# Kernel tuning notes

Hardware: AMD Instinct MI355X
Metric: run time of the kernel (lower is better)

## Reference

```python
import jax, jax.numpy as jnp
import numpy as np

N, C1, C2, H, W, NH = 4, 512, 512, 32, 32, 8


def _conv(x, w, pad):
    return jax.lax.conv_general_dilated(
        x, w, window_strides=(1, 1), padding=[(pad, pad), (pad, pad)],
        dimension_numbers=("NCHW", "OIHW", "NCHW"))


def _heads(t, n, c, nh):
    # [n, c, h, w] -> [n, nh, c, hw//nh] (spatial dim split across heads)
    return jnp.transpose(t.reshape(n, c, nh, -1), (0, 2, 1, 3))


def _attend(q, k, v):
    # q:[n,nh,Sq,d] k,v:[n,nh,Sk,d]; fp32 math as in the original
    scale = 1.0 / np.sqrt(k.shape[-1])
    att = jnp.einsum("nhqd,nhkd->nhqk", q.astype(jnp.float32), k.astype(jnp.float32)) * scale
    att = jax.nn.softmax(att, axis=-1)
    return jnp.einsum("nhqk,nhkd->nhqd", att, v.astype(jnp.float32))


def setup_inputs() -> dict:
    key = jax.random.key(0)
    ks = jax.random.split(key, 11)
    s = 0.02
    inp = {
        "x_l": jax.random.normal(ks[0], (N, C1, H, W), jnp.float32),
        "x_g": jax.random.normal(ks[1], (N, C2, H, W), jnp.float32),
        "Wk1": jax.random.normal(ks[2], (C1, C1, 3, 3), jnp.float32) * s,
        "Wq1": jax.random.normal(ks[3], (C1, C1, 3, 3), jnp.float32) * s,
        "Wv1": jax.random.normal(ks[4], (C1, C1, 3, 3), jnp.float32) * s,
        "Wk2": jax.random.normal(ks[5], (C2, C2, 3, 3), jnp.float32) * s,
        "Wq2": jax.random.normal(ks[6], (C2, C2, 3, 3), jnp.float32) * s,
        "Wv2": jax.random.normal(ks[7], (C2, C2, 3, 3), jnp.float32) * s,
        "Wp1": jax.random.normal(ks[8], (C1, C1, 1, 1), jnp.float32) * s,
        "Wp2": jax.random.normal(ks[9], (C2, C2, 1, 1), jnp.float32) * s,
        "resweight": jnp.ones((), jnp.float32),  # init 0 in torch; 1 used so the branch is active
    }
    return inp


def reference(x_l, x_g, Wk1, Wq1, Wv1, Wk2, Wq2, Wv2, Wp1, Wp2, resweight):
    n, c1, h, w = x_l.shape
    c2 = x_g.shape[1]
    k_l = _heads(_conv(x_l, Wk1, 1), n, c1, NH)
    q_l = _heads(_conv(x_l, Wq1, 1), n, c1, NH)
    v_l = _heads(_conv(x_l, Wv1, 1), n, c1, NH)
    k_g = _heads(_conv(x_g, Wk2, 1), n, c2, NH)
    q_g = _heads(_conv(x_g, Wq2, 1), n, c2, NH)
    v_g = _heads(_conv(x_g, Wv2, 1), n, c2, NH)

    # global queries attend over local keys/values
    y_g = _attend(q_g, k_l, v_l)                       # [n, nh, c2, hw/nh]
    y_g = jnp.transpose(y_g, (0, 2, 1, 3)).reshape(n, c2, h, w)
    y_g = _conv(y_g, Wp2, 0)

    # local queries attend over global keys/values
    y_l = _attend(q_l, k_g, v_g)                       # [n, nh, c1, hw/nh]
    y_l = jnp.transpose(y_l, (0, 2, 1, 3)).reshape(n, c1, h, w)
    y_l = _conv(y_l, Wp1, 0)

    return (x_l + y_l * resweight, x_g + y_g * resweight)
```

## Files before the change

kernel.cpp:

```cpp
#include <hip/hip_runtime.h>
#include <hip/hip_bf16.h>
#include <stdint.h>

typedef unsigned short u16;
typedef unsigned int u32;

#define TSLOT 2097152
#define IC_ELEMS 37748736ull
#define WB_ELEMS 14155776ull

typedef __attribute__((ext_vector_type(8))) short short8;
typedef __attribute__((ext_vector_type(8))) unsigned short u16x8;
typedef __attribute__((ext_vector_type(4))) float f32x4;

__device__ __forceinline__ float bf2f(u16 u) {
    union { u32 i; float f; } v; v.i = ((u32)u) << 16; return v.f;
}
__device__ __forceinline__ u16 f2bf(float f) {
    union { u32 i; float f; } v; v.f = f;
    u32 u = v.i;
    return (u16)((u + 0x7FFFu + ((u >> 16) & 1u)) >> 16);
}
__device__ __forceinline__ u32 pkbf(float a, float b) {
    __hip_bfloat162 h = __float22bfloat162_rn(make_float2(a, b));
    u32 u; __builtin_memcpy(&u, &h, 4); return u;
}

__device__ __forceinline__ void gl_lds16(const u16* g, u16* l) {
    __builtin_amdgcn_global_load_lds(
        (const __attribute__((address_space(1))) void*)(uintptr_t)(const void*)g,
        (__attribute__((address_space(3))) void*)(uintptr_t)(void*)l,
        16, 0, 0);
}

__global__ __launch_bounds__(256) void wconv_prep(
    const float* __restrict__ w0, const float* __restrict__ w1,
    const float* __restrict__ w2, const float* __restrict__ w3,
    const float* __restrict__ w4, const float* __restrict__ w5,
    u16* __restrict__ wbf)
{
    const int tsr = blockIdx.y;
    const float* src = tsr == 0 ? w0 : tsr == 1 ? w1 : tsr == 2 ? w2
                     : tsr == 3 ? w3 : tsr == 4 ? w4 : w5;
    const size_t base = (size_t)blockIdx.x * 4096 + threadIdx.x * 16;
    u16* dst = wbf + (size_t)tsr * 2359296 + base;
    const float4* s4 = (const float4*)(src + base);
    float4 f0 = s4[0], f1 = s4[1], f2 = s4[2], f3 = s4[3];
    u32 p[4];
    p[0] = pkbf(f0.x, f0.y); p[1] = pkbf(f0.z, f0.w);
    p[2] = pkbf(f1.x, f1.y); p[3] = pkbf(f1.z, f1.w);
    *(uint4*)dst = *(uint4*)p;
    p[0] = pkbf(f2.x, f2.y); p[1] = pkbf(f2.z, f2.w);
    p[2] = pkbf(f3.x, f3.y); p[3] = pkbf(f3.z, f3.w);
    *(uint4*)(dst + 8) = *(uint4*)p;
}

__global__ __launch_bounds__(256) void im2col_prep(
    const float* __restrict__ xl, const float* __restrict__ xg,
    u16* __restrict__ ic)
{
    __shared__ float xs[32][4][32];

    const int t  = threadIdx.x;
    const int mt = blockIdx.x;
    const int ct = blockIdx.y;
    const int m0 = mt * 64;
    const int img  = m0 >> 12;
    const int m_in = m0 & 4095;
    const int n_i  = m_in >> 10;
    const int y0   = (m_in & 1023) >> 5;

    const float* xp = (img ? xg : xl) + ((size_t)n_i * 512 + ct * 32) * 1024;

    for (int v = t; v < 4096; v += 256) {
        int ci = v >> 7;
        int r  = (v >> 5) & 3;
        int xx = v & 31;
        int yy = y0 - 1 + r;
        xs[ci][r][xx] = ((unsigned)yy < 32u) ? xp[ci * 1024 + yy * 32 + xx] : 0.f;
    }
    __syncthreads();

    const int m_local = t >> 2;
    const int q       = t & 3;
    const int y_sel   = m_local >> 5;
    const int x       = m_local & 31;
    u16* orow = ic + (size_t)(m0 + m_local) * 4608 + (size_t)(ct * 32 + q * 8) * 9;

    #pragma unroll
    for (int c = 0; c < 9; ++c) {
        u16x8 st;
        #pragma unroll
        for (int u = 0; u < 8; ++u) {
            const int e   = c * 8 + u;
            const int cil = q * 8 + e / 9;
            const int tap = e % 9;
            const int ky  = tap / 3, kx = tap % 3;
            int xx = x + kx - 1;
            float v = ((unsigned)xx < 32u) ? xs[cil][y_sel + ky][xx] : 0.f;
            st[u] = f2bf(v);
        }
        *(u16x8*)(orow + c * 8) = st;
    }
}

__global__ __launch_bounds__(256) void conv_gemm(
    const u16* __restrict__ ic, const u16* __restrict__ wbf,
    u16* __restrict__ kl, u16* __restrict__ ql, u16* __restrict__ vl,
    u16* __restrict__ kg, u16* __restrict__ qg, u16* __restrict__ vg)
{
    __shared__ u16 A_lds[128 * 64];
    __shared__ u16 B_lds[128 * 64];

    const int t  = threadIdx.x;
    const int mt = blockIdx.x;
    const int nt = blockIdx.y;
    const int img = mt >> 5;
    const int wt  = nt >> 2;
    const int co0 = (nt & 3) * 128;
    const int m0  = mt * 128;

    u16* osel = img == 0 ? (wt == 0 ? kl : wt == 1 ? ql : vl)
                         : (wt == 0 ? kg : wt == 1 ? qg : vg);
    const u16* wsel = wbf + (size_t)(img * 3 + wt) * 2359296;

    const int lane = t & 63;
    const int w4   = t >> 6;

    const int s_rb  = w4 * 8 + (lane >> 3);
    const int s_col = ((lane & 7) ^ (lane >> 3)) * 8;
    const u16* agp[4];
    const u16* bgp[4];
    #pragma unroll
    for (int i = 0; i < 4; ++i) {
        agp[i] = ic   + (size_t)(m0  + s_rb + i * 32) * 4608 + s_col;
        bgp[i] = wsel + (size_t)(co0 + s_rb + i * 32) * 4608 + s_col;
    }
    u16* Adst = A_lds + w4 * 512;
    u16* Bdst = B_lds + w4 * 512;

    const int wm = (w4 & 1) * 64;
    const int wn = (w4 >> 1) * 64;
    const int fr = lane & 15;
    const int qd = lane >> 4;
    int arow[4], brow[4];
    #pragma unroll
    for (int i = 0; i < 4; ++i) {
        arow[i] = wm + i * 16 + fr;
        brow[i] = wn + i * 16 + fr;
    }

    f32x4 acc[4][4] = {};

    for (int kb = 0; kb < 4608; kb += 64) {
        __syncthreads();
        #pragma unroll
        for (int i = 0; i < 4; ++i) {
            gl_lds16(agp[i] + kb, Adst + i * 2048);
            gl_lds16(bgp[i] + kb, Bdst + i * 2048);
        }
        __syncthreads();
        #pragma unroll
        for (int ks = 0; ks < 2; ++ks) {
            short8 af[4], bq[4];
            #pragma unroll
            for (int i = 0; i < 4; ++i) {
                int c = (ks * 4 + qd) ^ (arow[i] & 7);
                af[i] = *(const short8*)&A_lds[arow[i] * 64 + c * 8];
            }
            #pragma unroll
            for (int j = 0; j < 4; ++j) {
                int c = (ks * 4 + qd) ^ (brow[j] & 7);
                bq[j] = *(const short8*)&B_lds[brow[j] * 64 + c * 8];
            }
            #pragma unroll
            for (int i = 0; i < 4; ++i)
                #pragma unroll
                for (int j = 0; j < 4; ++j)
                    acc[i][j] = __builtin_amdgcn_mfma_f32_16x16x32_bf16(
                        af[i], bq[j], acc[i][j], 0, 0, 0);
        }
    }

    const int m_in = m0 & 4095;
    const int n_i  = m_in >> 10;
    const int head = (m_in & 1023) >> 7;
    u16* ob = osel + (size_t)(n_i * 8 + head) * 65536;
    if (wt == 2) {
        #pragma unroll
        for (int i = 0; i < 4; ++i) {
            int dd0 = wm + i * 16 + qd * 4;
            #pragma unroll
            for (int j = 0; j < 4; ++j) {
                int co = co0 + wn + j * 16 + fr;
                #pragma unroll
                for (int r = 0; r < 4; ++r)
                    ob[(size_t)(dd0 + r) * 512 + co] = f2bf(acc[i][j][r]);
            }
        }
    } else {
        #pragma unroll
        for (int i = 0; i < 4; ++i) {
            int dd0 = wm + i * 16 + qd * 4;
            #pragma unroll
            for (int j = 0; j < 4; ++j) {
                int co = co0 + wn + j * 16 + fr;
                ushort4 st;
                st.x = f2bf(acc[i][j][0]); st.y = f2bf(acc[i][j][1]);
                st.z = f2bf(acc[i][j][2]); st.w = f2bf(acc[i][j][3]);
                *(ushort4*)(ob + (size_t)co * 128 + dd0) = st;
            }
        }
    }
}

__global__ __launch_bounds__(256) void attn_mfma(
    const u16* __restrict__ Q0, const u16* __restrict__ K0,
    const u16* __restrict__ V0, u16* __restrict__ O0,
    const u16* __restrict__ Q1, const u16* __restrict__ K1,
    const u16* __restrict__ V1, u16* __restrict__ O1)
{
    __shared__ u16 Qs[64][136];
    __shared__ u16 Ks[64][136];
    __shared__ u16 Vs[128][72];
    __shared__ u16 Ps[64][72];

    const int t    = threadIdx.x;
    const int lane = t & 63;
    const int w    = t >> 6;
    const int qt   = blockIdx.x;
    const int nh   = blockIdx.y;
    const int z    = blockIdx.z;

    const u16* Q = (z ? Q1 : Q0) + (size_t)nh * 65536;
    const u16* K = (z ? K1 : K0) + (size_t)nh * 65536;
    const u16* V = (z ? V1 : V0) + (size_t)nh * 65536;
    u16*       O = (z ? O1 : O0) + (size_t)nh * 65536;

    const int q0 = qt * 64;
    for (int v = t; v < 1024; v += 256) {
        int row = v >> 4, c8 = (v & 15) * 8;
        *(u16x8*)&Qs[row][c8] = *(const u16x8*)(Q + (size_t)(q0 + row) * 128 + c8);
    }

    const int fr  = lane & 15;
    const int qd  = lane >> 4;
    const int koq = qd * 8;

    float m_run[4] = {-3e38f, -3e38f, -3e38f, -3e38f};
    float l_run[4] = {0.f, 0.f, 0.f, 0.f};
    f32x4 Ot[8] = {};
    const float scale = 0.08838834764831845f;

    for (int cb = 0; cb < 8; ++cb) {
        __syncthreads();
        const int kb = cb * 64;
        for (int v = t; v < 1024; v += 256) {
            int row = v >> 4, c8 = (v & 15) * 8;
            *(u16x8*)&Ks[row][c8] = *(const u16x8*)(K + (size_t)(kb + row) * 128 + c8);
        }
        for (int v = t; v < 1024; v += 256) {
            int row = v >> 3, c8 = (v & 7) * 8;
            *(u16x8*)&Vs[row][c8] = *(const u16x8*)(V + (size_t)row * 512 + kb + c8);
        }
        __syncthreads();

        f32x4 s[4] = {};
        #pragma unroll
        for (int dstep = 0; dstep < 4; ++dstep) {
            short8 a = *(const short8*)&Qs[w * 16 + fr][dstep * 32 + koq];
            #pragma unroll
            for (int nj = 0; nj < 4; ++nj) {
                short8 b = *(const short8*)&Ks[nj * 16 + fr][dstep * 32 + koq];
                s[nj] = __builtin_amdgcn_mfma_f32_16x16x32_bf16(a, b, s[nj], 0, 0, 0);
            }
        }

        float al[4];
        #pragma unroll
        for (int r = 0; r < 4; ++r) {
            float mc = fmaxf(fmaxf(s[0][r], s[1][r]), fmaxf(s[2][r], s[3][r])) * scale;
            mc = fmaxf(mc, __shfl_xor(mc, 1));
            mc = fmaxf(mc, __shfl_xor(mc, 2));
            mc = fmaxf(mc, __shfl_xor(mc, 4));
            mc = fmaxf(mc, __shfl_xor(mc, 8));
            float mn = fmaxf(m_run[r], mc);
            al[r] = __expf(m_run[r] - mn);
            m_run[r] = mn;
            float rs = 0.f;
            #pragma unroll
            for (int nj = 0; nj < 4; ++nj) {
                float p = __expf(s[nj][r] * scale - mn);
                s[nj][r] = p;
                rs += p;
            }
            rs += __shfl_xor(rs, 1);
            rs += __shfl_xor(rs, 2);
            rs += __shfl_xor(rs, 4);
            rs += __shfl_xor(rs, 8);
            l_run[r] = l_run[r] * al[r] + rs;
        }

        #pragma unroll
        for (int nj = 0; nj < 4; ++nj)
            #pragma unroll
            for (int r = 0; r < 4; ++r)
                Ps[w * 16 + qd * 4 + r][nj * 16 + fr] = f2bf(s[nj][r]);

        {
            int srcl = (fr >> 2) << 4;
            float a0 = __shfl(al[0], srcl), a1 = __shfl(al[1], srcl);
            float a2 = __shfl(al[2], srcl), a3 = __shfl(al[3], srcl);
            int rsel = fr & 3;
            float ac = rsel == 0 ? a0 : rsel == 1 ? a1 : rsel == 2 ? a2 : a3;
            #pragma unroll
            for (int t8 = 0; t8 < 8; ++t8)
                #pragma unroll
                for (int r = 0; r < 4; ++r)
                    Ot[t8][r] *= ac;
        }

        #pragma unroll
        for (int ks = 0; ks < 2; ++ks) {
            short8 b = *(const short8*)&Ps[w * 16 + fr][ks * 32 + koq];
            #pragma unroll
            for (int t8 = 0; t8 < 8; ++t8) {
                short8 a = *(const short8*)&Vs[t8 * 16 + fr][ks * 32 + koq];
                Ot[t8] = __builtin_amdgcn_mfma_f32_16x16x32_bf16(a, b, Ot[t8], 0, 0, 0);
            }
        }
    }

    int srcl = (fr >> 2) << 4;
    float l0 = __shfl(l_run[0], srcl), l1 = __shfl(l_run[1], srcl);
    float l2 = __shfl(l_run[2], srcl), l3 = __shfl(l_run[3], srcl);
    int rsel = fr & 3;
    float lc = rsel == 0 ? l0 : rsel == 1 ? l1 : rsel == 2 ? l2 : l3;
    float linv = 1.0f / lc;
    int c = q0 + w * 16 + fr;
    #pragma unroll
    for (int t8 = 0; t8 < 8; ++t8)
        #pragma unroll
        for (int r = 0; r < 4; ++r) {
            int d = t8 * 16 + qd * 4 + r;
            O[(size_t)d * 512 + c] = f2bf(Ot[t8][r] * linv);
        }
}

__global__ __launch_bounds__(256) void proj_mfma(
    const float* __restrict__ Wp1, const float* __restrict__ Wp2,
    const u16* __restrict__ Otl, const u16* __restrict__ Otg,
    const float* __restrict__ x_l, const float* __restrict__ x_g,
    const float* __restrict__ rwp,
    float* __restrict__ out0, float* __restrict__ out1)
{
    __shared__ u16 A_lds[128][40];
    __shared__ u16 B_lds[128][40];

    const int t  = threadIdx.x;
    const int ct = blockIdx.x;
    const int st = blockIdx.y;
    const int z  = blockIdx.z;
    const int which = z >> 2;
    const int nn    = z & 3;

    const float* Wp = which ? Wp2 : Wp1;
    const u16*   Ot = (which ? Otg : Otl) + (size_t)nn * 524288;
    const float* xr = (which ? x_g : x_l) + (size_t)nn * 524288;
    float*     outp = (which ? out1 : out0) + (size_t)nn * 524288;

    const int co0 = ct * 128, s0 = st * 128;
    const int row = t & 127, half = t >> 7;
    const float* wrow = Wp + (size_t)(co0 + row) * 512 + half * 16;
    const u16*   brow = Ot + (size_t)(s0 + row) * 512 + half * 16;

    const int lane = t & 63;
    const int wv4  = t >> 6;
    const int wm   = (wv4 & 1) * 64;
    const int wn   = (wv4 >> 1) * 64;
    const int fr   = lane & 15;
    const int koq  = (lane >> 4) * 8;

    f32x4 acc[4][4] = {};

    for (int kb = 0; kb < 512; kb += 32) {
        __syncthreads();
        {
            const float4* wp4 = (const float4*)(wrow + kb);
            float4 f0 = wp4[0], f1 = wp4[1], f2 = wp4[2], f3 = wp4[3];
            u32 p[4];
            p[0] = pkbf(f0.x, f0.y); p[1] = pkbf(f0.z, f0.w);
            p[2] = pkbf(f1.x, f1.y); p[3] = pkbf(f1.z, f1.w);
            *(uint4*)&A_lds[row][half * 16] = *(uint4*)p;
            p[0] = pkbf(f2.x, f2.y); p[1] = pkbf(f2.z, f2.w);
            p[2] = pkbf(f3.x, f3.y); p[3] = pkbf(f3.z, f3.w);
            *(uint4*)&A_lds[row][half * 16 + 8] = *(uint4*)p;
        }
        *(u16x8*)&B_lds[row][half * 16]     = *(const u16x8*)(brow + kb);
        *(u16x8*)&B_lds[row][half * 16 + 8] = *(const u16x8*)(brow + kb + 8);
        __syncthreads();
        short8 af[4], bf[4];
        #pragma unroll
        for (int i = 0; i < 4; ++i) af[i] = *(const short8*)&A_lds[wm + i * 16 + fr][koq];
        #pragma unroll
        for (int j = 0; j < 4; ++j) bf[j] = *(const short8*)&B_lds[wn + j * 16 + fr][koq];
        #pragma unroll
        for (int i = 0; i < 4; ++i)
            #pragma unroll
            for (int j = 0; j < 4; ++j)
                acc[i][j] = __builtin_amdgcn_mfma_f32_16x16x32_bf16(af[i], bf[j], acc[i][j], 0, 0, 0);
    }

    const float rwv = *rwp;
    #pragma unroll
    for (int i = 0; i < 4; ++i) {
        int co_b = co0 + wm + i * 16 + (lane >> 4) * 4;
        #pragma unroll
        for (int j = 0; j < 4; ++j) {
            int s = s0 + wn + j * 16 + fr;
            #pragma unroll
            for (int r = 0; r < 4; ++r) {
                size_t a = (size_t)(co_b + r) * 1024 + s;
                outp[a] = xr[a] + rwv * acc[i][j][r];
            }
        }
    }
}

extern "C" void kernel_launch(void* const* d_in, const int* in_sizes, int n_in,
                              void* d_out, int out_size, void* d_ws, size_t ws_size,
                              hipStream_t stream) {
    const float* x_l = (const float*)d_in[0];
    const float* x_g = (const float*)d_in[1];
    const float* Wk1 = (const float*)d_in[2];
    const float* Wq1 = (const float*)d_in[3];
    const float* Wv1 = (const float*)d_in[4];
    const float* Wk2 = (const float*)d_in[5];
    const float* Wq2 = (const float*)d_in[6];
    const float* Wv2 = (const float*)d_in[7];
    const float* Wp1 = (const float*)d_in[8];
    const float* Wp2 = (const float*)d_in[9];
    const float* rw  = (const float*)d_in[10];

    u16* ws  = (u16*)d_ws;
    u16* ic  = ws;
    u16* wbf = ws + IC_ELEMS;
    u16* Kl  = wbf + WB_ELEMS;
    u16* Ql  = Kl  + TSLOT;
    u16* Vtl = Ql  + TSLOT;
    u16* Kg  = Vtl + TSLOT;
    u16* Qg  = Kg  + TSLOT;
    u16* Vtg = Qg  + TSLOT;
    u16* Otg = Vtg + TSLOT;
    u16* Otl = Otg + TSLOT;

    float* out0 = (float*)d_out;
    float* out1 = out0 + (size_t)TSLOT;

    wconv_prep<<<dim3(576, 6), 256, 0, stream>>>(Wk1, Wq1, Wv1, Wk2, Wq2, Wv2, wbf);
    im2col_prep<<<dim3(128, 16), 256, 0, stream>>>(x_l, x_g, ic);

    conv_gemm<<<dim3(64, 12), 256, 0, stream>>>(
        ic, wbf, Kl, Ql, Vtl, Kg, Qg, Vtg);

    attn_mfma<<<dim3(8, 32, 2), 256, 0, stream>>>(
        Qg, Kl, Vtl, Otg, Ql, Kg, Vtg, Otl);

    proj_mfma<<<dim3(4, 8, 8), 256, 0, stream>>>(
        Wp1, Wp2, Otl, Otg, x_l, x_g, rw, out0, out1);
}
```

Measured before the change: 381.1 us.

## Merge prep kernels and use direct global-to-LDS loads in attention and projection

Merges the weight conversion and im2col prep kernels into one launch, and adds a conversion of the projection weights to bf16 there. The attention and projection kernels now stage tiles with global_load_lds into XOR-swizzled LDS layouts instead of register round-trips through padded arrays. The projection K-step doubles to 64. This aims to remove one launch, the in-loop fp32-to-bf16 conversion, and LDS staging overhead. It adds more workspace use and requires the swizzle indexing to be correct.

```diff
diff --git a/kernel.cpp b/kernel.cpp
--- a/kernel.cpp
+++ b/kernel.cpp
@@ -8,6 +8,7 @@
 #define TSLOT 2097152
 #define IC_ELEMS 37748736ull
 #define WB_ELEMS 14155776ull
+#define WPB_ELEMS 524288ull
 
 typedef __attribute__((ext_vector_type(8))) short short8;
 typedef __attribute__((ext_vector_type(8))) unsigned short u16x8;
@@ -33,37 +34,55 @@
         16, 0, 0);
 }
 
-__global__ __launch_bounds__(256) void wconv_prep(
+__global__ __launch_bounds__(256) void prep_all(
+    const float* __restrict__ xl, const float* __restrict__ xg,
     const float* __restrict__ w0, const float* __restrict__ w1,
     const float* __restrict__ w2, const float* __restrict__ w3,
     const float* __restrict__ w4, const float* __restrict__ w5,
-    u16* __restrict__ wbf)
-{
-    const int tsr = blockIdx.y;
-    const float* src = tsr == 0 ? w0 : tsr == 1 ? w1 : tsr == 2 ? w2
-                     : tsr == 3 ? w3 : tsr == 4 ? w4 : w5;
-    const size_t base = (size_t)blockIdx.x * 4096 + threadIdx.x * 16;
-    u16* dst = wbf + (size_t)tsr * 2359296 + base;
-    const float4* s4 = (const float4*)(src + base);
-    float4 f0 = s4[0], f1 = s4[1], f2 = s4[2], f3 = s4[3];
-    u32 p[4];
-    p[0] = pkbf(f0.x, f0.y); p[1] = pkbf(f0.z, f0.w);
-    p[2] = pkbf(f1.x, f1.y); p[3] = pkbf(f1.z, f1.w);
-    *(uint4*)dst = *(uint4*)p;
-    p[0] = pkbf(f2.x, f2.y); p[1] = pkbf(f2.z, f2.w);
-    p[2] = pkbf(f3.x, f3.y); p[3] = pkbf(f3.z, f3.w);
-    *(uint4*)(dst + 8) = *(uint4*)p;
-}
-
-__global__ __launch_bounds__(256) void im2col_prep(
-    const float* __restrict__ xl, const float* __restrict__ xg,
-    u16* __restrict__ ic)
+    const float* __restrict__ wp1, const float* __restrict__ wp2,
+    u16* __restrict__ wbf, u16* __restrict__ ic, u16* __restrict__ wpb)
 {
     __shared__ float xs[32][4][32];
-
-    const int t  = threadIdx.x;
-    const int mt = blockIdx.x;
-    const int ct = blockIdx.y;
+    const int b = blockIdx.x;
+    const int t = threadIdx.x;
+
+    if (b < 3456) {
+        const int tsr = b / 576, inner = b - tsr * 576;
+        const float* src = tsr == 0 ? w0 : tsr == 1 ? w1 : tsr == 2 ? w2
+                         : tsr == 3 ? w3 : tsr == 4 ? w4 : w5;
+        const size_t base = (size_t)inner * 4096 + t * 16;
+        u16* dst = wbf + (size_t)tsr * 2359296 + base;
+        const float4* s4 = (const float4*)(src + base);
+        float4 f0 = s4[0], f1 = s4[1], f2 = s4[2], f3 = s4[3];
+        u32 p[4];
+        p[0] = pkbf(f0.x, f0.y); p[1] = pkbf(f0.z, f0.w);
+        p[2] = pkbf(f1.x, f1.y); p[3] = pkbf(f1.z, f1.w);
+        *(uint4*)dst = *(uint4*)p;
+        p[0] = pkbf(f2.x, f2.y); p[1] = pkbf(f2.z, f2.w);
+        p[2] = pkbf(f3.x, f3.y); p[3] = pkbf(f3.z, f3.w);
+        *(uint4*)(dst + 8) = *(uint4*)p;
+        return;
+    }
+    if (b >= 5504) {
+        const int b3 = b - 5504;
+        const float* src = (b3 < 64) ? wp1 : wp2;
+        const size_t base = (size_t)(b3 & 63) * 4096 + t * 16;
+        u16* dst = wpb + ((b3 < 64) ? 0 : 262144) + base;
+        const float4* s4 = (const float4*)(src + base);
+        float4 f0 = s4[0], f1 = s4[1], f2 = s4[2], f3 = s4[3];
+        u32 p[4];
+        p[0] = pkbf(f0.x, f0.y); p[1] = pkbf(f0.z, f0.w);
+        p[2] = pkbf(f1.x, f1.y); p[3] = pkbf(f1.z, f1.w);
+        *(uint4*)dst = *(uint4*)p;
+        p[0] = pkbf(f2.x, f2.y); p[1] = pkbf(f2.z, f2.w);
+        p[2] = pkbf(f3.x, f3.y); p[3] = pkbf(f3.z, f3.w);
+        *(uint4*)(dst + 8) = *(uint4*)p;
+        return;
+    }
+
+    const int b2 = b - 3456;
+    const int mt = b2 >> 4;
+    const int ct = b2 & 15;
     const int m0 = mt * 64;
     const int img  = m0 >> 12;
     const int m_in = m0 & 4095;
@@ -109,8 +128,8 @@
     u16* __restrict__ kl, u16* __restrict__ ql, u16* __restrict__ vl,
     u16* __restrict__ kg, u16* __restrict__ qg, u16* __restrict__ vg)
 {
-    __shared__ u16 A_lds[128 * 64];
-    __shared__ u16 B_lds[128 * 64];
+    __shared__ __align__(16) u16 A_lds[128 * 64];
+    __shared__ __align__(16) u16 B_lds[128 * 64];
 
     const int t  = threadIdx.x;
     const int mt = blockIdx.x;
@@ -220,9 +239,11 @@
     const u16* __restrict__ Q1, const u16* __restrict__ K1,
     const u16* __restrict__ V1, u16* __restrict__ O1)
 {
-    __shared__ u16 Qs[64][136];
-    __shared__ u16 Ks[64][136];
-    __shared__ u16 Vs[128][72];
+    __shared__ __align__(16) u16 Qlo[64 * 64];
+    __shared__ __align__(16) u16 Qhi[64 * 64];
+    __shared__ __align__(16) u16 Klo[64 * 64];
+    __shared__ __align__(16) u16 Khi[64 * 64];
+    __shared__ __align__(16) u16 Vs[128 * 64];
     __shared__ u16 Ps[64][72];
 
     const int t    = threadIdx.x;
@@ -237,10 +258,20 @@
     const u16* V = (z ? V1 : V0) + (size_t)nh * 65536;
     u16*       O = (z ? O1 : O0) + (size_t)nh * 65536;
 
-    const int q0 = qt * 64;
-    for (int v = t; v < 1024; v += 256) {
-        int row = v >> 4, c8 = (v & 15) * 8;
-        *(u16x8*)&Qs[row][c8] = *(const u16x8*)(Q + (size_t)(q0 + row) * 128 + c8);
+    const int q0    = qt * 64;
+    const int s_rb  = w * 8 + (lane >> 3);
+    const int s_col = ((lane & 7) ^ (lane >> 3)) * 8;
+    u16* const dQl = Qlo + w * 512;
+    u16* const dQh = Qhi + w * 512;
+    u16* const dKl = Klo + w * 512;
+    u16* const dKh = Khi + w * 512;
+    u16* const dV  = Vs  + w * 512;
+
+    #pragma unroll
+    for (int i = 0; i < 2; ++i) {
+        const u16* qr = Q + (size_t)(q0 + s_rb + i * 32) * 128;
+        gl_lds16(qr + s_col,      dQl + i * 2048);
+        gl_lds16(qr + 64 + s_col, dQh + i * 2048);
     }
 
     const int fr  = lane & 15;
@@ -255,23 +286,27 @@
     for (int cb = 0; cb < 8; ++cb) {
         __syncthreads();
         const int kb = cb * 64;
-        for (int v = t; v < 1024; v += 256) {
-            int row = v >> 4, c8 = (v & 15) * 8;
-            *(u16x8*)&Ks[row][c8] = *(const u16x8*)(K + (size_t)(kb + row) * 128 + c8);
-        }
-        for (int v = t; v < 1024; v += 256) {
-            int row = v >> 3, c8 = (v & 7) * 8;
-            *(u16x8*)&Vs[row][c8] = *(const u16x8*)(V + (size_t)row * 512 + kb + c8);
-        }
+        #pragma unroll
+        for (int i = 0; i < 2; ++i) {
+            const u16* kr = K + (size_t)(kb + s_rb + i * 32) * 128;
+            gl_lds16(kr + s_col,      dKl + i * 2048);
+            gl_lds16(kr + 64 + s_col, dKh + i * 2048);
+        }
+        #pragma unroll
+        for (int i = 0; i < 4; ++i)
+            gl_lds16(V + (size_t)(s_rb + i * 32) * 512 + kb + s_col, dV + i * 2048);
         __syncthreads();
 
         f32x4 s[4] = {};
         #pragma unroll
         for (int dstep = 0; dstep < 4; ++dstep) {
-            short8 a = *(const short8*)&Qs[w * 16 + fr][dstep * 32 + koq];
+            const u16* Qh = (dstep < 2) ? Qlo : Qhi;
+            const u16* Kh = (dstep < 2) ? Klo : Khi;
+            const int cq = (((dstep & 1) * 4 + qd) ^ (fr & 7)) * 8;
+            short8 a = *(const short8*)&Qh[(w * 16 + fr) * 64 + cq];
             #pragma unroll
             for (int nj = 0; nj < 4; ++nj) {
-                short8 b = *(const short8*)&Ks[nj * 16 + fr][dstep * 32 + koq];
+                short8 b = *(const short8*)&Kh[(nj * 16 + fr) * 64 + cq];
                 s[nj] = __builtin_amdgcn_mfma_f32_16x16x32_bf16(a, b, s[nj], 0, 0, 0);
             }
         }
@@ -325,7 +360,8 @@
             short8 b = *(const short8*)&Ps[w * 16 + fr][ks * 32 + koq];
             #pragma unroll
             for (int t8 = 0; t8 < 8; ++t8) {
-                short8 a = *(const short8*)&Vs[t8 * 16 + fr][ks * 32 + koq];
+                const int cv = ((ks * 4 + qd) ^ (fr & 7)) * 8;
+                short8 a = *(const short8*)&Vs[(t8 * 16 + fr) * 64 + cv];
                 Ot[t8] = __builtin_amdgcn_mfma_f32_16x16x32_bf16(a, b, Ot[t8], 0, 0, 0);
             }
         }
@@ -348,14 +384,14 @@
 }
 
 __global__ __launch_bounds__(256) void proj_mfma(
-    const float* __restrict__ Wp1, const float* __restrict__ Wp2,
+    const u16* __restrict__ wpb,
     const u16* __restrict__ Otl, const u16* __restrict__ Otg,
     const float* __restrict__ x_l, const float* __restrict__ x_g,
     const float* __restrict__ rwp,
     float* __restrict__ out0, float* __restrict__ out1)
 {
-    __shared__ u16 A_lds[128][40];
-    __shared__ u16 B_lds[128][40];
+    __shared__ __align__(16) u16 A_lds[128 * 64];
+    __shared__ __align__(16) u16 B_lds[128 * 64];
 
     const int t  = threadIdx.x;
     const int ct = blockIdx.x;
@@ -364,57 +400,74 @@
     const int which = z >> 2;
     const int nn    = z & 3;
 
-    const float* Wp = which ? Wp2 : Wp1;
+    const u16*   Wp = wpb + (which ? 262144 : 0);
     const u16*   Ot = (which ? Otg : Otl) + (size_t)nn * 524288;
     const float* xr = (which ? x_g : x_l) + (size_t)nn * 524288;
     float*     outp = (which ? out1 : out0) + (size_t)nn * 524288;
 
     const int co0 = ct * 128, s0 = st * 128;
-    const int row = t & 127, half = t >> 7;
-    const float* wrow = Wp + (size_t)(co0 + row) * 512 + half * 16;
-    const u16*   brow = Ot + (size_t)(s0 + row) * 512 + half * 16;
-
     const int lane = t & 63;
-    const int wv4  = t >> 6;
-    const int wm   = (wv4 & 1) * 64;
-    const int wn   = (wv4 >> 1) * 64;
-    const int fr   = lane & 15;
-    const int koq  = (lane >> 4) * 8;
+    const int w4   = t >> 6;
+
+    const int s_rb  = w4 * 8 + (lane >> 3);
+    const int s_col = ((lane & 7) ^ (lane >> 3)) * 8;
+    const u16* agp[4];
+    const u16* bgp[4];
+    #pragma unroll
+    for (int i = 0; i < 4; ++i) {
+        agp[i] = Wp + (size_t)(co0 + s_rb + i * 32) * 512 + s_col;
+        bgp[i] = Ot + (size_t)(s0  + s_rb + i * 32) * 512 + s_col;
+    }
+    u16* Adst = A_lds + w4 * 512;
+    u16* Bdst = B_lds + w4 * 512;
+
+    const int wm = (w4 & 1) * 64;
+    const int wn = (w4 >> 1) * 64;
+    const int fr = lane & 15;
+    const int qd = lane >> 4;
+    int arow[4], brow[4];
+    #pragma unroll
+    for (int i = 0; i < 4; ++i) {
+        arow[i] = wm + i * 16 + fr;
+        brow[i] = wn + i * 16 + fr;
+    }
 
     f32x4 acc[4][4] = {};
 
-    for (int kb = 0; kb < 512; kb += 32) {
+    for (int kb = 0; kb < 512; kb += 64) {
         __syncthreads();
-        {
-            const float4* wp4 = (const float4*)(wrow + kb);
-            float4 f0 = wp4[0], f1 = wp4[1], f2 = wp4[2], f3 = wp4[3];
-            u32 p[4];
-            p[0] = pkbf(f0.x, f0.y); p[1] = pkbf(f0.z, f0.w);
-            p[2] = pkbf(f1.x, f1.y); p[3] = pkbf(f1.z, f1.w);
-            *(uint4*)&A_lds[row][half * 16] = *(uint4*)p;
-            p[0] = pkbf(f2.x, f2.y); p[1] = pkbf(f2.z, f2.w);
-            p[2] = pkbf(f3.x, f3.y); p[3] = pkbf(f3.z, f3.w);
-            *(uint4*)&A_lds[row][half * 16 + 8] = *(uint4*)p;
-        }
-        *(u16x8*)&B_lds[row][half * 16]     = *(const u16x8*)(brow + kb);
-        *(u16x8*)&B_lds[row][half * 16 + 8] = *(const u16x8*)(brow + kb + 8);
+        #pragma unroll
+        for (int i = 0; i < 4; ++i) {
+            gl_lds16(agp[i] + kb, Adst + i * 2048);
+            gl_lds16(bgp[i] + kb, Bdst + i * 2048);
+        }
         __syncthreads();
-        short8 af[4], bf[4];
-        #pragma unroll
-        for (int i = 0; i < 4; ++i) af[i] = *(const short8*)&A_lds[wm + i * 16 + fr][koq];
-        #pragma unroll
-        for (int j = 0; j < 4; ++j) bf[j] = *(const short8*)&B_lds[wn + j * 16 + fr][koq];
-        #pragma unroll
-        for (int i = 0; i < 4; ++i)
-            #pragma unroll
-            for (int j = 0; j < 4; ++j)
-                acc[i][j] = __builtin_amdgcn_mfma_f32_16x16x32_bf16(af[i], bf[j], acc[i][j], 0, 0, 0);
+        #pragma unroll
+        for (int ks = 0; ks < 2; ++ks) {
+            short8 af[4], bq[4];
+            #pragma unroll
+            for (int i = 0; i < 4; ++i) {
+                int c = (ks * 4 + qd) ^ (arow[i] & 7);
+                af[i] = *(const short8*)&A_lds[arow[i] * 64 + c * 8];
+            }
+            #pragma unroll
+            for (int j = 0; j < 4; ++j) {
+                int c = (ks * 4 + qd) ^ (brow[j] & 7);
+                bq[j] = *(const short8*)&B_lds[brow[j] * 64 + c * 8];
+            }
+            #pragma unroll
+            for (int i = 0; i < 4; ++i)
+                #pragma unroll
+                for (int j = 0; j < 4; ++j)
+                    acc[i][j] = __builtin_amdgcn_mfma_f32_16x16x32_bf16(
+                        af[i], bq[j], acc[i][j], 0, 0, 0);
+        }
     }
 
     const float rwv = *rwp;
     #pragma unroll
     for (int i = 0; i < 4; ++i) {
-        int co_b = co0 + wm + i * 16 + (lane >> 4) * 4;
+        int co_b = co0 + wm + i * 16 + qd * 4;
         #pragma unroll
         for (int j = 0; j < 4; ++j) {
             int s = s0 + wn + j * 16 + fr;
@@ -453,12 +506,13 @@
     u16* Vtg = Qg  + TSLOT;
     u16* Otg = Vtg + TSLOT;
     u16* Otl = Otg + TSLOT;
+    u16* wpb = Otl + TSLOT;
 
     float* out0 = (float*)d_out;
     float* out1 = out0 + (size_t)TSLOT;
 
-    wconv_prep<<<dim3(576, 6), 256, 0, stream>>>(Wk1, Wq1, Wv1, Wk2, Wq2, Wv2, wbf);
-    im2col_prep<<<dim3(128, 16), 256, 0, stream>>>(x_l, x_g, ic);
+    prep_all<<<5632, 256, 0, stream>>>(
+        x_l, x_g, Wk1, Wq1, Wv1, Wk2, Wq2, Wv2, Wp1, Wp2, wbf, ic, wpb);
 
     conv_gemm<<<dim3(64, 12), 256, 0, stream>>>(
         ic, wbf, Kl, Ql, Vtl, Kg, Qg, Vtg);
@@ -467,5 +521,5 @@
         Qg, Kl, Vtl, Otg, Ql, Kg, Vtg, Otl);
 
     proj_mfma<<<dim3(4, 8, 8), 256, 0, stream>>>(
-        Wp1, Wp2, Otl, Otg, x_l, x_g, rw, out0, out1);
-}
+        wpb, Otl, Otg, x_l, x_g, rw, out0, out1);
+}
```

Measured after the change: 348.8 us. 8.5% less time.
